# Kernel optimization log

Measured on AMD Instinct MI355X. Metric: run time of the kernel, lower is better.

The kernel has to match this reference:

```python
import jax, jax.numpy as jnp
import numpy as np

B, T, D, U = 64, 4096, 256, 64

def setup_inputs() -> dict:
    key = jax.random.key(0)
    k1, k2, k3 = jax.random.split(key, 3)
    inputs = jax.random.normal(k1, (B, T, D), dtype=jnp.float32)
    # glorot_uniform init for W (D,U) and u (U,1); zeros bias
    limW = float(np.sqrt(6.0 / (D + U)))
    W = jax.random.uniform(k2, (D, U), minval=-limW, maxval=limW, dtype=jnp.float32)
    limu = float(np.sqrt(6.0 / (U + 1)))
    u = jax.random.uniform(k3, (U, 1), minval=-limu, maxval=limu, dtype=jnp.float32)
    b = jnp.zeros((U,), dtype=jnp.float32)
    return {"inputs": inputs, "W": W, "b": b, "u": u}

def reference(inputs, W, b, u):
    # score: [B,T,U] = tanh(inputs @ W + b)
    score = jnp.tanh(jnp.einsum('btd,du->btu', inputs, W) + b)
    # logits: [B,T,1]; softmax over time axis (axis=1)
    logits = jnp.einsum('btu,uo->bto', score, u)
    attention_weights = jax.nn.softmax(logits, axis=1)
    # weighted sum over time -> [B,D]
    context = jnp.sum(inputs * attention_weights, axis=1)
    return (context, attention_weights)
```

## Files before the change

kernel.cpp:

```cpp
#include <hip/hip_runtime.h>
#include <math.h>

#define B_ 64
#define T_ 4096
#define D_ 256
#define U_ 64
#define RPB 32
#define NPB (T_ / RPB)
#define XPAD 264

typedef float f32x4 __attribute__((ext_vector_type(4)));
typedef short bf16x8 __attribute__((ext_vector_type(8)));

__device__ __forceinline__ unsigned short f2bf_rne(float f) {
    unsigned u = __float_as_uint(f);
    unsigned r = u + 0x7fffu + ((u >> 16) & 1u);
    return (unsigned short)(r >> 16);
}
__device__ __forceinline__ float bfbits2f(unsigned short s) {
    return __uint_as_float(((unsigned)s) << 16);
}

__global__ __launch_bounds__(256) void wprep_kernel(
    const float* __restrict__ W, unsigned short* __restrict__ whi,
    unsigned short* __restrict__ wlo)
{
    int fi = blockIdx.x * 256 + threadIdx.x;
    int j    = fi & 7;
    int lane = (fi >> 3) & 63;
    int tile = fi >> 9;
    int nt = tile & 3, ks = tile >> 2;
    int k = ks * 32 + (lane >> 4) * 8 + j;
    int n = nt * 16 + (lane & 15);
    float w = W[k * U_ + n];
    unsigned short hi = f2bf_rne(w);
    unsigned short lo = f2bf_rne(w - bfbits2f(hi));
    whi[fi] = hi;
    wlo[fi] = lo;
}

__global__ __launch_bounds__(256, 4) void fused_main(
    const float* __restrict__ x, const unsigned short* __restrict__ whi,
    const unsigned short* __restrict__ wlo, const float* __restrict__ bias,
    const float* __restrict__ uvec, float* __restrict__ wts,
    float* __restrict__ Zp, float* __restrict__ Pp)
{
    __shared__ unsigned short Ahi[RPB * XPAD];
    __shared__ unsigned short Alo[RPB * XPAD];
    __shared__ float part[RPB][4];

    int tid = threadIdx.x;
    int lane = tid & 63, wid = tid >> 6;
    int q = lane >> 4, r = lane & 15;

    int b = blockIdx.x / NPB;
    int pb = blockIdx.x % NPB;
    size_t row00 = (size_t)b * T_ + (size_t)pb * RPB;

    int col = wid * 16 + r;
    float bv = bias[col], uv = uvec[col];

    {
        const float4* xs4 = (const float4*)(x + row00 * D_);
        float4 xs[8];
#pragma unroll
        for (int i = 0; i < 8; ++i) xs[i] = xs4[tid + i * 256];
#pragma unroll
        for (int i = 0; i < 8; ++i) {
            int f = tid + i * 256;
            int row = f >> 6, c4 = f & 63;
            float4 v = xs[i];
            unsigned short h0 = f2bf_rne(v.x), h1 = f2bf_rne(v.y),
                           h2 = f2bf_rne(v.z), h3 = f2bf_rne(v.w);
            unsigned short l0 = f2bf_rne(v.x - bfbits2f(h0)),
                           l1 = f2bf_rne(v.y - bfbits2f(h1)),
                           l2 = f2bf_rne(v.z - bfbits2f(h2)),
                           l3 = f2bf_rne(v.w - bfbits2f(h3));
            int base = row * XPAD + c4 * 4;
            uint2 hp = { (unsigned)h0 | ((unsigned)h1 << 16),
                         (unsigned)h2 | ((unsigned)h3 << 16) };
            uint2 lp = { (unsigned)l0 | ((unsigned)l1 << 16),
                         (unsigned)l2 | ((unsigned)l3 << 16) };
            *(uint2*)(&Ahi[base]) = hp;
            *(uint2*)(&Alo[base]) = lp;
        }
    }
    __syncthreads();

    bf16x8 Bh[8], Bl[8];
    {
        const bf16x8* whiV = (const bf16x8*)whi;
        const bf16x8* wloV = (const bf16x8*)wlo;
#pragma unroll
        for (int ks = 0; ks < 8; ++ks) {
            Bh[ks] = whiV[(ks * 4 + wid) * 64 + lane];
            Bl[ks] = wloV[(ks * 4 + wid) * 64 + lane];
        }
    }

#pragma unroll
    for (int s = 0; s < 2; ++s) {
        f32x4 acc = (f32x4){0.f, 0.f, 0.f, 0.f};
        int arow = (s * 16 + r) * XPAD + q * 8;
#pragma unroll
        for (int ks = 0; ks < 8; ++ks) {
            bf16x8 ahi = *(const bf16x8*)(&Ahi[arow + ks * 32]);
            bf16x8 alo = *(const bf16x8*)(&Alo[arow + ks * 32]);
            acc = __builtin_amdgcn_mfma_f32_16x16x32_bf16(ahi, Bh[ks], acc, 0, 0, 0);
            acc = __builtin_amdgcn_mfma_f32_16x16x32_bf16(ahi, Bl[ks], acc, 0, 0, 0);
            acc = __builtin_amdgcn_mfma_f32_16x16x32_bf16(alo, Bh[ks], acc, 0, 0, 0);
        }
        float p0 = fmaf(1.f - 2.f / (__expf(2.f * (acc[0] + bv)) + 1.f), uv, 0.f);
        float p1 = fmaf(1.f - 2.f / (__expf(2.f * (acc[1] + bv)) + 1.f), uv, 0.f);
        float p2 = fmaf(1.f - 2.f / (__expf(2.f * (acc[2] + bv)) + 1.f), uv, 0.f);
        float p3 = fmaf(1.f - 2.f / (__expf(2.f * (acc[3] + bv)) + 1.f), uv, 0.f);
#pragma unroll
        for (int off = 1; off < 16; off <<= 1) {
            p0 += __shfl_xor(p0, off, 64);
            p1 += __shfl_xor(p1, off, 64);
            p2 += __shfl_xor(p2, off, 64);
            p3 += __shfl_xor(p3, off, 64);
        }
        if (r == 0) {
            int row = s * 16 + q * 4;
            part[row + 0][wid] = p0;
            part[row + 1][wid] = p1;
            part[row + 2][wid] = p2;
            part[row + 3][wid] = p3;
        }
    }
    __syncthreads();

    int colg = tid & 31, ph = tid >> 5;
    float ew[4];
#pragma unroll
    for (int j = 0; j < 4; ++j) {
        int row = j * 8 + ph;
        float lg = (part[row][0] + part[row][1]) + (part[row][2] + part[row][3]);
        ew[j] = __expf(lg);
    }
    if (wid == 0 && lane < RPB) {
        float lg = (part[lane][0] + part[lane][1]) + (part[lane][2] + part[lane][3]);
        float e = __expf(lg);
        wts[row00 + lane] = e;
        float z = e;
#pragma unroll
        for (int off = 1; off < 32; off <<= 1) z += __shfl_xor(z, off, 32);
        if (lane == 0) Zp[blockIdx.x] = z;
    }

    float pacc[8];
#pragma unroll
    for (int j = 0; j < 8; ++j) pacc[j] = 0.f;
#pragma unroll
    for (int i = 0; i < 4; ++i) {
        int row = i * 8 + ph;
        float w = ew[i];
        union { uint4 u; unsigned short sh[8]; } v;
        v.u = *(const uint4*)(&Ahi[row * XPAD + colg * 8]);
#pragma unroll
        for (int j = 0; j < 8; ++j)
            pacc[j] = fmaf(w, bfbits2f(v.sh[j]), pacc[j]);
    }
    float* red = (float*)Alo;
#pragma unroll
    for (int j = 0; j < 8; ++j) red[ph * 256 + colg * 8 + j] = pacc[j];
    __syncthreads();
    float ssum = 0.f;
#pragma unroll
    for (int p = 0; p < 8; ++p) ssum += red[p * 256 + tid];
    Pp[(size_t)blockIdx.x * D_ + tid] = ssum;
}

__global__ __launch_bounds__(256) void finalize_kernel(
    float* __restrict__ wts, const float* __restrict__ Zp,
    const float* __restrict__ Pp, float* __restrict__ ctx)
{
    int b = blockIdx.x;
    int tid = threadIdx.x;
    float Z = 0.f;
#pragma unroll 8
    for (int i = 0; i < NPB; ++i) Z += Zp[b * NPB + i];
    float invZ = 1.f / Z;

    float s = 0.f;
#pragma unroll 4
    for (int i = 0; i < NPB; ++i) s += Pp[(size_t)(b * NPB + i) * D_ + tid];
    ctx[b * D_ + tid] = s * invZ;

    float4* wp = (float4*)(wts + (size_t)b * T_);
#pragma unroll
    for (int i = 0; i < T_ / 4 / 256; ++i) {
        float4 v = wp[tid + i * 256];
        v.x *= invZ; v.y *= invZ; v.z *= invZ; v.w *= invZ;
        wp[tid + i * 256] = v;
    }
}

extern "C" void kernel_launch(void* const* d_in, const int* in_sizes, int n_in,
                              void* d_out, int out_size, void* d_ws, size_t ws_size,
                              hipStream_t stream) {
    const float* x    = (const float*)d_in[0];
    const float* W    = (const float*)d_in[1];
    const float* bias = (const float*)d_in[2];
    const float* uvec = (const float*)d_in[3];

    float* out = (float*)d_out;
    float* ctx = out;
    float* wts = out + B_ * D_;

    unsigned short* whi = (unsigned short*)d_ws;
    unsigned short* wlo = whi + D_ * U_;
    float* Zp = (float*)(wlo + D_ * U_);
    float* Pp = Zp + B_ * NPB;

    wprep_kernel<<<D_ * U_ / 256, 256, 0, stream>>>(W, whi, wlo);
    fused_main<<<(B_ * T_) / RPB, 256, 0, stream>>>(x, whi, wlo, bias, uvec, wts, Zp, Pp);
    finalize_kernel<<<B_, 256, 0, stream>>>(wts, Zp, Pp, ctx);
}
```

Baseline: 390.4 us.

## Stage x tile via direct global-to-LDS loads and split finalize across more blocks

The main kernel now copies the fp32 x tile straight into shared memory with global_load_lds DMA. It then reads the tile back into registers to split it into bf16 hi/lo halves, and the W fragment loads are moved ahead of this. The aim is to cut register pressure and let loads bypass VGPRs, at the cost of an extra LDS round trip and two more barriers. The finalize kernel is split into four blocks per batch so its partial-sum reduction and weight normalization run with more parallelism.

```diff
diff --git a/kernel.cpp b/kernel.cpp
--- a/kernel.cpp
+++ b/kernel.cpp
@@ -45,9 +45,12 @@
     const float* __restrict__ uvec, float* __restrict__ wts,
     float* __restrict__ Zp, float* __restrict__ Pp)
 {
-    __shared__ unsigned short Ahi[RPB * XPAD];
-    __shared__ unsigned short Alo[RPB * XPAD];
+    __shared__ __align__(16) unsigned char smem[RPB * XPAD * 4];
     __shared__ float part[RPB][4];
+
+    unsigned short* Ahi = (unsigned short*)smem;
+    unsigned short* Alo = (unsigned short*)(smem + RPB * XPAD * 2);
+    float* xf = (float*)smem;
 
     int tid = threadIdx.x;
     int lane = tid & 63, wid = tid >> 6;
@@ -59,33 +62,6 @@
 
     int col = wid * 16 + r;
     float bv = bias[col], uv = uvec[col];
-
-    {
-        const float4* xs4 = (const float4*)(x + row00 * D_);
-        float4 xs[8];
-#pragma unroll
-        for (int i = 0; i < 8; ++i) xs[i] = xs4[tid + i * 256];
-#pragma unroll
-        for (int i = 0; i < 8; ++i) {
-            int f = tid + i * 256;
-            int row = f >> 6, c4 = f & 63;
-            float4 v = xs[i];
-            unsigned short h0 = f2bf_rne(v.x), h1 = f2bf_rne(v.y),
-                           h2 = f2bf_rne(v.z), h3 = f2bf_rne(v.w);
-            unsigned short l0 = f2bf_rne(v.x - bfbits2f(h0)),
-                           l1 = f2bf_rne(v.y - bfbits2f(h1)),
-                           l2 = f2bf_rne(v.z - bfbits2f(h2)),
-                           l3 = f2bf_rne(v.w - bfbits2f(h3));
-            int base = row * XPAD + c4 * 4;
-            uint2 hp = { (unsigned)h0 | ((unsigned)h1 << 16),
-                         (unsigned)h2 | ((unsigned)h3 << 16) };
-            uint2 lp = { (unsigned)l0 | ((unsigned)l1 << 16),
-                         (unsigned)l2 | ((unsigned)l3 << 16) };
-            *(uint2*)(&Ahi[base]) = hp;
-            *(uint2*)(&Alo[base]) = lp;
-        }
-    }
-    __syncthreads();
 
     bf16x8 Bh[8], Bl[8];
     {
@@ -97,6 +73,47 @@
             Bl[ks] = wloV[(ks * 4 + wid) * 64 + lane];
         }
     }
+
+    {
+        const float* gbase = x + row00 * D_;
+#pragma unroll
+        for (int i = 0; i < 8; ++i) {
+            int chunk = wid * 8 + i;
+            const void* gp = (const void*)(gbase + chunk * 256 + lane * 4);
+            void* lp = (void*)(xf + chunk * 256);
+            __builtin_amdgcn_global_load_lds(
+                (const __attribute__((address_space(1))) void*)gp,
+                (__attribute__((address_space(3))) void*)lp, 16, 0, 0);
+        }
+    }
+    __syncthreads();
+
+    f32x4 xs[8];
+#pragma unroll
+    for (int i = 0; i < 8; ++i)
+        xs[i] = *(const f32x4*)(xf + (size_t)(tid + i * 256) * 4);
+    __syncthreads();
+
+#pragma unroll
+    for (int i = 0; i < 8; ++i) {
+        int f = tid + i * 256;
+        int row = f >> 6, c4 = f & 63;
+        f32x4 v = xs[i];
+        unsigned short h0 = f2bf_rne(v[0]), h1 = f2bf_rne(v[1]),
+                       h2 = f2bf_rne(v[2]), h3 = f2bf_rne(v[3]);
+        unsigned short l0 = f2bf_rne(v[0] - bfbits2f(h0)),
+                       l1 = f2bf_rne(v[1] - bfbits2f(h1)),
+                       l2 = f2bf_rne(v[2] - bfbits2f(h2)),
+                       l3 = f2bf_rne(v[3] - bfbits2f(h3));
+        int base = row * XPAD + c4 * 4;
+        uint2 hp = { (unsigned)h0 | ((unsigned)h1 << 16),
+                     (unsigned)h2 | ((unsigned)h3 << 16) };
+        uint2 lp = { (unsigned)l0 | ((unsigned)l1 << 16),
+                     (unsigned)l2 | ((unsigned)l3 << 16) };
+        *(uint2*)(&Ahi[base]) = hp;
+        *(uint2*)(&Alo[base]) = lp;
+    }
+    __syncthreads();
 
 #pragma unroll
     for (int s = 0; s < 2; ++s) {
@@ -176,25 +193,32 @@
     float* __restrict__ wts, const float* __restrict__ Zp,
     const float* __restrict__ Pp, float* __restrict__ ctx)
 {
-    int b = blockIdx.x;
+    __shared__ float red2[4][64];
+    int bp = blockIdx.x;
+    int b = bp >> 2, p = bp & 3;
     int tid = threadIdx.x;
+
     float Z = 0.f;
 #pragma unroll 8
     for (int i = 0; i < NPB; ++i) Z += Zp[b * NPB + i];
     float invZ = 1.f / Z;
 
+    int c = tid & 63, g = tid >> 6;
     float s = 0.f;
 #pragma unroll 4
-    for (int i = 0; i < NPB; ++i) s += Pp[(size_t)(b * NPB + i) * D_ + tid];
-    ctx[b * D_ + tid] = s * invZ;
-
-    float4* wp = (float4*)(wts + (size_t)b * T_);
-#pragma unroll
-    for (int i = 0; i < T_ / 4 / 256; ++i) {
-        float4 v = wp[tid + i * 256];
-        v.x *= invZ; v.y *= invZ; v.z *= invZ; v.w *= invZ;
-        wp[tid + i * 256] = v;
-    }
+    for (int i = 0; i < 32; ++i)
+        s += Pp[(size_t)(b * NPB + g * 32 + i) * D_ + p * 64 + c];
+    red2[g][c] = s;
+    __syncthreads();
+    if (tid < 64) {
+        float t = (red2[0][tid] + red2[1][tid]) + (red2[2][tid] + red2[3][tid]);
+        ctx[b * D_ + p * 64 + tid] = t * invZ;
+    }
+
+    float4* wp = (float4*)(wts + (size_t)b * T_ + (size_t)p * 1024);
+    float4 v = wp[tid];
+    v.x *= invZ; v.y *= invZ; v.z *= invZ; v.w *= invZ;
+    wp[tid] = v;
 }
 
 extern "C" void kernel_launch(void* const* d_in, const int* in_sizes, int n_in,
@@ -216,5 +240,5 @@
 
     wprep_kernel<<<D_ * U_ / 256, 256, 0, stream>>>(W, whi, wlo);
     fused_main<<<(B_ * T_) / RPB, 256, 0, stream>>>(x, whi, wlo, bias, uvec, wts, Zp, Pp);
-    finalize_kernel<<<B_, 256, 0, stream>>>(wts, Zp, Pp, ctx);
-}
+    finalize_kernel<<<B_ * 4, 256, 0, stream>>>(wts, Zp, Pp, ctx);
+}
```

New measurement: 368.3 us. 1.06x faster.
